# Kernel tuning notes

Measured on AMD Instinct MI355X. Metric: run time of the kernel, lower is better.

Reference implementation:

```python
import jax, jax.numpy as jnp
import numpy as np

N = 100000   # nodes
E = 3200000  # edges (before self-loops)
F = 128      # input feature dim
H = 2        # heads
C = 16       # hidden per head
G = 64       # graphs in batch
NEG_SLOPE = 0.2


def _gat_layer(x, src, dst, eattr, W, a_src, a_dst, W_e, a_e, bias):
    # x: [N, Fin]; W: [Fin, H*C]; eattr: [Et, 1]; W_e: [1, H*C]; a_*: [H, C]
    n = x.shape[0]
    h = (x @ W).reshape(n, H, C)                      # [N,H,C]
    asrc = jnp.sum(h * a_src, axis=-1)                # [N,H]
    adst = jnp.sum(h * a_dst, axis=-1)                # [N,H]
    he = (eattr @ W_e).reshape(-1, H, C)              # [Et,H,C]
    aedge = jnp.sum(he * a_e, axis=-1)                # [Et,H]
    alpha = jax.nn.leaky_relu(asrc[src] + adst[dst] + aedge, NEG_SLOPE)
    # segment softmax over incoming edges of each destination node
    m = jax.ops.segment_max(alpha, dst, num_segments=n)
    ex = jnp.exp(alpha - m[dst])
    s = jax.ops.segment_sum(ex, dst, num_segments=n)
    att = ex / (s[dst] + 1e-16)                        # [Et,H]
    msg = h[src] * att[:, :, None]                     # [Et,H,C]
    out = jax.ops.segment_sum(msg, dst, num_segments=n)  # [N,H,C]
    return out.reshape(n, H * C) + bias


def setup_inputs() -> dict:
    key = jax.random.key(0)
    ks = jax.random.split(key, 24)
    d = {
        'x': jax.random.normal(ks[0], (N, F), dtype=jnp.float32),
        'edge_index': jax.random.randint(ks[1], (2, E), 0, N, dtype=jnp.int64),
        'edge_attr': jax.random.normal(ks[2], (E, 1), dtype=jnp.float32),
        'batch': jnp.sort(jax.random.randint(ks[3], (N,), 0, G, dtype=jnp.int64)),
        # conv1: F -> H*C
        'W1': jax.random.normal(ks[4], (F, H * C), dtype=jnp.float32) * 0.1,
        'att_src1': jax.random.normal(ks[5], (H, C), dtype=jnp.float32) * 0.1,
        'att_dst1': jax.random.normal(ks[6], (H, C), dtype=jnp.float32) * 0.1,
        'We1': jax.random.normal(ks[7], (1, H * C), dtype=jnp.float32) * 0.1,
        'att_edge1': jax.random.normal(ks[8], (H, C), dtype=jnp.float32) * 0.1,
        'b1': jnp.zeros((H * C,), dtype=jnp.float32),
        # conv2: H*C -> H*C
        'W2': jax.random.normal(ks[9], (H * C, H * C), dtype=jnp.float32) * 0.1,
        'att_src2': jax.random.normal(ks[10], (H, C), dtype=jnp.float32) * 0.1,
        'att_dst2': jax.random.normal(ks[11], (H, C), dtype=jnp.float32) * 0.1,
        'We2': jax.random.normal(ks[12], (1, H * C), dtype=jnp.float32) * 0.1,
        'att_edge2': jax.random.normal(ks[13], (H, C), dtype=jnp.float32) * 0.1,
        'b2': jnp.zeros((H * C,), dtype=jnp.float32),
        # predictor MLP: 32 -> 32 -> 2
        'Wf1': jax.random.normal(ks[14], (H * C, 32), dtype=jnp.float32) * 0.1,
        'bf1': jnp.zeros((32,), dtype=jnp.float32),
        'Wf2': jax.random.normal(ks[15], (32, 2), dtype=jnp.float32) * 0.1,
        'bf2': jnp.zeros((2,), dtype=jnp.float32),
    }
    return d


def reference(x, edge_index, edge_attr, batch,
              W1, att_src1, att_dst1, We1, att_edge1, b1,
              W2, att_src2, att_dst2, We2, att_edge2, b2,
              Wf1, bf1, Wf2, bf2):
    n = x.shape[0]
    # PyG GATConv default: add self-loops with edge_attr fill_value='mean'
    loops = jnp.arange(n, dtype=edge_index.dtype)
    src = jnp.concatenate([edge_index[0], loops])
    dst = jnp.concatenate([edge_index[1], loops])
    ea = jnp.concatenate([edge_attr,
                          jnp.broadcast_to(edge_attr.mean(axis=0, keepdims=True), (n, 1))])
    h = _gat_layer(x, src, dst, ea, W1, att_src1, att_dst1, We1, att_edge1, b1)
    h = jax.nn.relu(h)  # dropout is identity in eval mode
    h = _gat_layer(h, src, dst, ea, W2, att_src2, att_dst2, We2, att_edge2, b2)
    # global mean pool over graphs
    sums = jax.ops.segment_sum(h, batch, num_segments=G)          # [G, H*C]
    cnt = jax.ops.segment_sum(jnp.ones((n,), h.dtype), batch, num_segments=G)
    emb = sums / jnp.maximum(cnt, 1.0)[:, None]
    # predictor MLP
    return jax.nn.relu(emb @ Wf1 + bf1) @ Wf2 + bf2               # [G, 2]
```

## Files before the change

kernel.cpp:

```cpp
#include <hip/hip_runtime.h>
#include <hip/hip_fp16.h>

#define N_NODES 100000
#define N_EDGES 3200000
#define F_IN    128
#define HC      32
#define CH      16
#define NGRAPH  64
#define NEG     0.2f

#define BSH   8
#define BNODE (1 << BSH)
#define NB2   ((N_NODES + BNODE - 1) >> BSH)
#define CAP   9216
#define EPB   4096
#define BTHR  1024
#define GPAD  16
#define CHK   4096
#define NPB   512
#define GSPAN 16

__device__ __forceinline__ float lrelu(float x) { return x > 0.f ? x : NEG * x; }

__device__ __forceinline__ int wscan(int v) {
#pragma unroll
    for (int off = 1; off < 64; off <<= 1) {
        int u = __shfl_up(v, off, 64);
        if ((int)(threadIdx.x & 63) >= off) v += u;
    }
    return v;
}


__global__ void k_init(int* __restrict__ gcur, float* __restrict__ params,
                       float* __restrict__ gsums) {
    int t = threadIdx.x;
    if (t < NB2) gcur[t * GPAD] = t * CAP;
    if (t < 16) params[t] = 0.f;
    gsums[t] = 0.f;
    gsums[t + 1024] = 0.f;
}


__global__ __launch_bounds__(1024)
void k_bucket(const int* __restrict__ src, const int* __restrict__ dst,
              const float* __restrict__ ea, int* __restrict__ gcur,
              int2* __restrict__ staged, float* __restrict__ params) {
    __shared__ int lcur[NB2];
    __shared__ int lscan[512];
    __shared__ int gbase[NB2];
    __shared__ int wsum[8];
    __shared__ short rbkt[EPB];
    __shared__ int2 recs[EPB];
    int t = threadIdx.x;
    int base = blockIdx.x * EPB;
    float acc = 0.f;
    for (int i = t; i < NB2; i += BTHR) lcur[i] = 0;
    __syncthreads();
    int  myb[EPB / BTHR];
    int  myrank[EPB / BTHR];
    int2 myrec[EPB / BTHR];
#pragma unroll
    for (int i = 0; i < EPB / BTHR; ++i) {
        int e = base + i * BTHR + t;
        myb[i] = -1;
        if (e < N_EDGES) {
            int dv = dst[e];
            float eav = ea[e];
            acc += eav;
            myb[i] = dv >> BSH;
            myrank[i] = atomicAdd(&lcur[myb[i]], 1);
            myrec[i] = make_int2((src[e] << BSH) | (dv & (BNODE - 1)),
                                 __float_as_int(eav));
        }
    }
    __syncthreads();
    int v = 0;
    if (t < 512) v = (t < NB2) ? lcur[t] : 0;
    int sv = wscan(v);
    if (t < 512 && (t & 63) == 63) wsum[t >> 6] = sv;
    if (t < NB2 && lcur[t] > 0) gbase[t] = atomicAdd(&gcur[t * GPAD], lcur[t]);
    __syncthreads();
    if (t < 512) {
        int bb = 0;
        for (int i = 0; i < (t >> 6); ++i) bb += wsum[i];
        lscan[t] = sv + bb;
    }
    __syncthreads();
#pragma unroll
    for (int i = 0; i < EPB / BTHR; ++i) {
        if (myb[i] >= 0) {
            int p = lscan[myb[i]] - lcur[myb[i]] + myrank[i];
            recs[p] = myrec[i];
            rbkt[p] = (short)myb[i];
        }
    }
    __syncthreads();
    int tot = lscan[511];
    for (int p = t; p < tot; p += BTHR) {
        int b = rbkt[p];
        int ex = lscan[b] - lcur[b];
        staged[gbase[b] + (p - ex)] = recs[p];
    }
    for (int m = 32; m >= 1; m >>= 1) acc += __shfl_xor(acc, m, 64);
    __shared__ float sh[BTHR / 64];
    int lane = t & 63, wid = t >> 6;
    if (lane == 0) sh[wid] = acc;
    __syncthreads();
    if (t == 0) {
        float s = 0.f;
        for (int i = 0; i < BTHR / 64; ++i) s += sh[i];
        unsafeAtomicAdd(&params[0], s);
    }
}


__global__ void k_setup(const float* __restrict__ We1, const float* __restrict__ ae1,
                        const float* __restrict__ We2, const float* __restrict__ ae2,
                        float* __restrict__ params, const int* __restrict__ gcur,
                        int* __restrict__ gstart, int* __restrict__ rowptr) {
    int t = threadIdx.x;
    if (t < 2) {
        float c1 = 0.f, c2 = 0.f;
        for (int c = 0; c < CH; ++c) {
            c1 += We1[t * CH + c] * ae1[t * CH + c];
            c2 += We2[t * CH + c] * ae2[t * CH + c];
        }
        params[2 + t] = c1;
        params[4 + t] = c2;
        if (t == 0) params[1] = params[0] / (float)N_EDGES;
    }
    __shared__ int sh[256];
    int v[2];
    int s = 0;
    for (int j = 0; j < 2; ++j) {
        int i = t * 2 + j;
        v[j] = (i < NB2) ? (gcur[i * GPAD] - i * CAP) : 0;
        s += v[j];
    }
    sh[t] = s;
    __syncthreads();
    for (int off = 1; off < 256; off <<= 1) {
        int u = (t >= off) ? sh[t - off] : 0;
        __syncthreads();
        sh[t] += u;
        __syncthreads();
    }
    int ex = sh[t] - s;
    for (int j = 0; j < 2; ++j) {
        int i = t * 2 + j;
        if (i < NB2) { gstart[i] = ex; ex += v[j]; }
    }
    if (t == 255) {
        gstart[NB2] = N_EDGES;
        rowptr[N_NODES] = N_EDGES;
    }
}


__global__ __launch_bounds__(1024)
void k_scatter(const int2* __restrict__ staged, const int* __restrict__ gcur,
               const int* __restrict__ gstart,
               int* __restrict__ rowptr, int* __restrict__ eidx,
               __half* __restrict__ eea) {
    __shared__ int cntl[BNODE];
    __shared__ int cur[BNODE];
    __shared__ int cchist[BNODE];
    __shared__ int cexcl[BNODE];
    __shared__ int ws4[4];
    __shared__ short rbkt[CHK];
    __shared__ int2 recs[CHK];
    int b = blockIdx.x, t = threadIdx.x;
    int nbase = b << BSH;
    int bcount = N_NODES - nbase;
    if (bcount > BNODE) bcount = BNODE;
    int sbase = b * CAP;
    int en = gcur[b * GPAD];
    int st_true = gstart[b];
    if (t < BNODE) cntl[t] = 0;
    __syncthreads();
    for (int e = sbase + t; e < en; e += 1024)
        atomicAdd(&cntl[staged[e].x & (BNODE - 1)], 1);
    __syncthreads();
    {
        int v = (t < BNODE) ? cntl[t] : 0;
        int sv = wscan(v);
        if (t < BNODE && (t & 63) == 63) ws4[t >> 6] = sv;
        __syncthreads();
        if (t < BNODE) {
            int bb = 0;
            for (int i = 0; i < (t >> 6); ++i) bb += ws4[i];
            int ex = st_true + sv + bb - v;
            cur[t] = ex;
            if (t < bcount) rowptr[nbase + t] = ex;
        }
        __syncthreads();
    }
    int count = en - sbase;
    for (int cb = 0; cb < count; cb += CHK) {
        int clen = count - cb;
        if (clen > CHK) clen = CHK;
        if (t < BNODE) cchist[t] = 0;
        __syncthreads();
        int  mylo[CHK / 1024];
        int  myrank[CHK / 1024];
        int2 myrec[CHK / 1024];
#pragma unroll
        for (int i = 0; i < CHK / 1024; ++i) {
            int p = i * 1024 + t;
            mylo[i] = -1;
            if (p < clen) {
                int2 r = staged[sbase + cb + p];
                mylo[i] = r.x & (BNODE - 1);
                myrank[i] = atomicAdd(&cchist[mylo[i]], 1);
                myrec[i] = r;
            }
        }
        __syncthreads();
        {
            int v = (t < BNODE) ? cchist[t] : 0;
            int sv = wscan(v);
            if (t < BNODE && (t & 63) == 63) ws4[t >> 6] = sv;
            __syncthreads();
            if (t < BNODE) {
                int bb = 0;
                for (int i = 0; i < (t >> 6); ++i) bb += ws4[i];
                cexcl[t] = sv + bb - v;
            }
            __syncthreads();
        }
#pragma unroll
        for (int i = 0; i < CHK / 1024; ++i) {
            if (mylo[i] >= 0) {
                int p = cexcl[mylo[i]] + myrank[i];
                recs[p] = myrec[i];
                rbkt[p] = (short)mylo[i];
            }
        }
        __syncthreads();
        for (int p = t; p < clen; p += 1024) {
            int lo = rbkt[p];
            int pos = cur[lo] + (p - cexcl[lo]);
            int2 r = recs[p];
            eidx[pos] = r.x;
            eea[pos] = __float2half(__int_as_float(r.y));
        }
        __syncthreads();
        if (t < BNODE) cur[t] += cchist[t];
        __syncthreads();
    }
}


#define COLS(ac, xv)                                                     \
    ac[0] = fmaf(xv.x, w0.x, ac[0]); ac[1] = fmaf(xv.x, w0.y, ac[1]);    \
    ac[2] = fmaf(xv.x, w0.z, ac[2]); ac[3] = fmaf(xv.x, w0.w, ac[3]);    \
    ac[0] = fmaf(xv.y, w1.x, ac[0]); ac[1] = fmaf(xv.y, w1.y, ac[1]);    \
    ac[2] = fmaf(xv.y, w1.z, ac[2]); ac[3] = fmaf(xv.y, w1.w, ac[3]);    \
    ac[0] = fmaf(xv.z, w2.x, ac[0]); ac[1] = fmaf(xv.z, w2.y, ac[1]);    \
    ac[2] = fmaf(xv.z, w2.z, ac[2]); ac[3] = fmaf(xv.z, w2.w, ac[3]);    \
    ac[0] = fmaf(xv.w, w3.x, ac[0]); ac[1] = fmaf(xv.w, w3.y, ac[1]);    \
    ac[2] = fmaf(xv.w, w3.z, ac[2]); ac[3] = fmaf(xv.w, w3.w, ac[3]);

template <int FIN>
__global__ __launch_bounds__(256)
void k_linear(const float* __restrict__ x, const float* __restrict__ W,
              const float* __restrict__ a_src, const float* __restrict__ a_dst,
              __half* __restrict__ h16, float* __restrict__ asrc,
              float* __restrict__ adst) {
    constexpr int PAD = FIN + 4;
    __shared__ float ws[FIN * HC];
    __shared__ float xs[64 * PAD];
    int t = threadIdx.x;
    int nbase = blockIdx.x * 64;
    int bcount = N_NODES - nbase;
    if (bcount > 64) bcount = 64;

    for (int i = t; i < FIN * HC / 4; i += 256)
        ((float4*)ws)[i] = ((const float4*)W)[i];
    const float4* xg = (const float4*)(x + (size_t)nbase * FIN);
    int nf4 = bcount * FIN / 4;
    for (int i = t; i < 64 * FIN / 4; i += 256) {
        if (i < nf4) {
            float4 v = xg[i];
            int flat = i * 4;
            int row = flat / FIN, col = flat % FIN;
            *(float4*)&xs[row * PAD + col] = v;
        }
    }
    __syncthreads();

    int cg = t & 7, np = t >> 3;
    int n0 = np * 2, n1 = n0 + 1;
    float acc0[4] = {0.f, 0.f, 0.f, 0.f};
    float acc1[4] = {0.f, 0.f, 0.f, 0.f};
#pragma unroll
    for (int k = 0; k < FIN; k += 4) {
        float4 xa = *(const float4*)&xs[n0 * PAD + k];
        float4 xb = *(const float4*)&xs[n1 * PAD + k];
        const float4* wp = (const float4*)&ws[k * HC] + cg;
        float4 w0 = wp[0], w1 = wp[8], w2 = wp[16], w3 = wp[24];
        COLS(acc0, xa)
        COLS(acc1, xb)
    }

    int hh = cg >> 2;
    float s0 = 0.f, d0 = 0.f, s1 = 0.f, d1 = 0.f;
#pragma unroll
    for (int j = 0; j < 4; ++j) {
        float av = a_src[hh * CH + (cg & 3) * 4 + j];
        float dv = a_dst[hh * CH + (cg & 3) * 4 + j];
        s0 = fmaf(acc0[j], av, s0); d0 = fmaf(acc0[j], dv, d0);
        s1 = fmaf(acc1[j], av, s1); d1 = fmaf(acc1[j], dv, d1);
    }
    s0 += __shfl_xor(s0, 1, 64); s0 += __shfl_xor(s0, 2, 64);
    d0 += __shfl_xor(d0, 1, 64); d0 += __shfl_xor(d0, 2, 64);
    s1 += __shfl_xor(s1, 1, 64); s1 += __shfl_xor(s1, 2, 64);
    d1 += __shfl_xor(d1, 1, 64); d1 += __shfl_xor(d1, 2, 64);

    if (n0 < bcount) {
        __half2 pa = __floats2half2_rn(acc0[0], acc0[1]);
        __half2 pb = __floats2half2_rn(acc0[2], acc0[3]);
        *(uint2*)&h16[(size_t)(nbase + n0) * HC + cg * 4] =
            make_uint2(*(unsigned*)&pa, *(unsigned*)&pb);
        if ((cg & 3) == 0) {
            asrc[(nbase + n0) * 2 + hh] = s0;
            adst[(nbase + n0) * 2 + hh] = d0;
        }
    }
    if (n1 < bcount) {
        __half2 pa = __floats2half2_rn(acc1[0], acc1[1]);
        __half2 pb = __floats2half2_rn(acc1[2], acc1[3]);
        *(uint2*)&h16[(size_t)(nbase + n1) * HC + cg * 4] =
            make_uint2(*(unsigned*)&pa, *(unsigned*)&pb);
        if ((cg & 3) == 0) {
            asrc[(nbase + n1) * 2 + hh] = s1;
            adst[(nbase + n1) * 2 + hh] = d1;
        }
    }
}


#define FMA4(ACC, WGT, VEC)                                                      \
    ACC.x = fmaf(WGT, VEC.x, ACC.x); ACC.y = fmaf(WGT, VEC.y, ACC.y);            \
    ACC.z = fmaf(WGT, VEC.z, ACC.z); ACC.w = fmaf(WGT, VEC.w, ACC.w);

__device__ __forceinline__ void unpack8(uint4 hv, float4& p, float4& u) {
    float2 f0 = __half22float2(*(__half2*)&hv.x);
    float2 f1 = __half22float2(*(__half2*)&hv.y);
    float2 f2 = __half22float2(*(__half2*)&hv.z);
    float2 f3 = __half22float2(*(__half2*)&hv.w);
    p = make_float4(f0.x, f0.y, f1.x, f1.y);
    u = make_float4(f2.x, f2.y, f3.x, f3.y);
}

template <int FUSE>
__global__ __launch_bounds__(256)
void k_gat(const int* __restrict__ rowptr, const int* __restrict__ eidx,
           const __half* __restrict__ eea, const __half* __restrict__ h16,
           const float* __restrict__ asrc, const float* __restrict__ adst,
           const float* __restrict__ params, int ceoff,
           const float* __restrict__ bias, int do_relu,
           float* __restrict__ outf, __half* __restrict__ outh,
           const float* __restrict__ W2,
           const float* __restrict__ as2, const float* __restrict__ ad2,
           float* __restrict__ asrc2, float* __restrict__ adst2) {
    __shared__ float w2s[FUSE ? HC * HC : 4];
    int t = threadIdx.x;
    if (FUSE) {
        for (int i = t; i < HC * HC / 4; i += 256)
            ((float4*)w2s)[i] = ((const float4*)W2)[i];
        __syncthreads();
    }
    int tid = blockIdx.x * blockDim.x + t;
    int n = tid >> 4;
    if (n >= N_NODES) return;
    int q = tid & 15;
    int chan = q & 3, quarter = q >> 2, hh = chan >> 1;
    int st = rowptr[n], en = rowptr[n + 1];
    int len = en - st;
    int q0 = st + ((len * quarter) >> 2);
    int q1 = st + ((len * (quarter + 1)) >> 2);
    float ce = params[ceoff + hh];
    float adn = adst[n * 2 + hh];
    const uint4* h4v = (const uint4*)h16;
    float4 A0 = make_float4(0.f, 0.f, 0.f, 0.f);
    float4 A1 = make_float4(0.f, 0.f, 0.f, 0.f);
    float ssum = 0.f;
    for (int e = q0; e < q1; e += 4) {
        int e1 = e + 1, e2 = e + 2, e3 = e + 3;
        int i1 = e1 < q1 ? e1 : q1 - 1;
        int i2 = e2 < q1 ? e2 : q1 - 1;
        int i3 = e3 < q1 ? e3 : q1 - 1;
        int r0 = eidx[e], r1 = eidx[i1], r2 = eidx[i2], r3 = eidx[i3];
        float ea0 = __half2float(eea[e]),  ea1 = __half2float(eea[i1]);
        float ea2 = __half2float(eea[i2]), ea3 = __half2float(eea[i3]);
        int s0 = r0 >> BSH, s1 = r1 >> BSH, s2 = r2 >> BSH, s3 = r3 >> BSH;
        float a0 = asrc[s0 * 2 + hh], a1 = asrc[s1 * 2 + hh];
        float a2 = asrc[s2 * 2 + hh], a3 = asrc[s3 * 2 + hh];
        uint4 hv0 = h4v[s0 * 4 + chan];
        uint4 hv1 = h4v[s1 * 4 + chan];
        uint4 hv2 = h4v[s2 * 4 + chan];
        uint4 hv3 = h4v[s3 * 4 + chan];
        float g0 = __expf(lrelu(a0 + adn + ce * ea0));
        float g1 = __expf(lrelu(a1 + adn + ce * ea1));
        float g2 = __expf(lrelu(a2 + adn + ce * ea2));
        float g3 = __expf(lrelu(a3 + adn + ce * ea3));
        g1 = (e1 < q1) ? g1 : 0.f;
        g2 = (e2 < q1) ? g2 : 0.f;
        g3 = (e3 < q1) ? g3 : 0.f;
        float4 p0, u0, p1, u1, p2, u2, p3, u3;
        unpack8(hv0, p0, u0); unpack8(hv1, p1, u1);
        unpack8(hv2, p2, u2); unpack8(hv3, p3, u3);
        FMA4(A0, g0, p0) FMA4(A1, g0, u0) ssum += g0;
        FMA4(A0, g1, p1) FMA4(A1, g1, u1) ssum += g1;
        FMA4(A0, g2, p2) FMA4(A1, g2, u2) ssum += g2;
        FMA4(A0, g3, p3) FMA4(A1, g3, u3) ssum += g3;
    }
    if (quarter == 0) {
        float gself = __expf(lrelu(asrc[n * 2 + hh] + adn + ce * params[1]));
        float4 psf, usf;
        unpack8(h4v[n * 4 + chan], psf, usf);
        FMA4(A0, gself, psf) FMA4(A1, gself, usf)
        ssum += gself;
    }
    A0.x += __shfl_xor(A0.x, 4, 64); A0.y += __shfl_xor(A0.y, 4, 64);
    A0.z += __shfl_xor(A0.z, 4, 64); A0.w += __shfl_xor(A0.w, 4, 64);
    A1.x += __shfl_xor(A1.x, 4, 64); A1.y += __shfl_xor(A1.y, 4, 64);
    A1.z += __shfl_xor(A1.z, 4, 64); A1.w += __shfl_xor(A1.w, 4, 64);
    ssum += __shfl_xor(ssum, 4, 64);
    A0.x += __shfl_xor(A0.x, 8, 64); A0.y += __shfl_xor(A0.y, 8, 64);
    A0.z += __shfl_xor(A0.z, 8, 64); A0.w += __shfl_xor(A0.w, 8, 64);
    A1.x += __shfl_xor(A1.x, 8, 64); A1.y += __shfl_xor(A1.y, 8, 64);
    A1.z += __shfl_xor(A1.z, 8, 64); A1.w += __shfl_xor(A1.w, 8, 64);
    ssum += __shfl_xor(ssum, 8, 64);
    if (quarter != 0) return;
    float inv = 1.f / (ssum + 1e-16f);
    int b4 = chan * 2;
    float4 bv0 = ((const float4*)bias)[b4], bv1 = ((const float4*)bias)[b4 + 1];
    float4 v0 = make_float4(A0.x * inv + bv0.x, A0.y * inv + bv0.y,
                            A0.z * inv + bv0.z, A0.w * inv + bv0.w);
    float4 v1 = make_float4(A1.x * inv + bv1.x, A1.y * inv + bv1.y,
                            A1.z * inv + bv1.z, A1.w * inv + bv1.w);
    if (do_relu) {
        v0.x = fmaxf(v0.x, 0.f); v0.y = fmaxf(v0.y, 0.f);
        v0.z = fmaxf(v0.z, 0.f); v0.w = fmaxf(v0.w, 0.f);
        v1.x = fmaxf(v1.x, 0.f); v1.y = fmaxf(v1.y, 0.f);
        v1.z = fmaxf(v1.z, 0.f); v1.w = fmaxf(v1.w, 0.f);
    }
    if (!FUSE) {
        ((float4*)outf)[n * 8 + b4] = v0;
        ((float4*)outf)[n * 8 + b4 + 1] = v1;
        return;
    }
    int lane = t & 63;
    int bse = lane & 48;
    float h2[8] = {0.f, 0.f, 0.f, 0.f, 0.f, 0.f, 0.f, 0.f};
#pragma unroll
    for (int cc = 0; cc < 4; ++cc) {
        int sl = bse | cc;
        float vv[8];
        vv[0] = __shfl(v0.x, sl, 64); vv[1] = __shfl(v0.y, sl, 64);
        vv[2] = __shfl(v0.z, sl, 64); vv[3] = __shfl(v0.w, sl, 64);
        vv[4] = __shfl(v1.x, sl, 64); vv[5] = __shfl(v1.y, sl, 64);
        vv[6] = __shfl(v1.z, sl, 64); vv[7] = __shfl(v1.w, sl, 64);
#pragma unroll
        for (int m = 0; m < 8; ++m) {
            const float* wrow = &w2s[(cc * 8 + m) * HC + chan * 8];
            float4 wa = *(const float4*)&wrow[0];
            float4 wb = *(const float4*)&wrow[4];
            h2[0] = fmaf(vv[m], wa.x, h2[0]); h2[1] = fmaf(vv[m], wa.y, h2[1]);
            h2[2] = fmaf(vv[m], wa.z, h2[2]); h2[3] = fmaf(vv[m], wa.w, h2[3]);
            h2[4] = fmaf(vv[m], wb.x, h2[4]); h2[5] = fmaf(vv[m], wb.y, h2[5]);
            h2[6] = fmaf(vv[m], wb.z, h2[6]); h2[7] = fmaf(vv[m], wb.w, h2[7]);
        }
    }
    __half2 q0h = __floats2half2_rn(h2[0], h2[1]);
    __half2 q1h = __floats2half2_rn(h2[2], h2[3]);
    __half2 q2h = __floats2half2_rn(h2[4], h2[5]);
    __half2 q3h = __floats2half2_rn(h2[6], h2[7]);
    *(uint4*)&outh[(size_t)n * HC + chan * 8] =
        make_uint4(*(unsigned*)&q0h, *(unsigned*)&q1h,
                   *(unsigned*)&q2h, *(unsigned*)&q3h);
    float s2 = 0.f, d2 = 0.f;
#pragma unroll
    for (int j = 0; j < 8; ++j) {
        s2 = fmaf(h2[j], as2[chan * 8 + j], s2);
        d2 = fmaf(h2[j], ad2[chan * 8 + j], d2);
    }
    s2 += __shfl_xor(s2, 1, 64);
    d2 += __shfl_xor(d2, 1, 64);
    if ((chan & 1) == 0) {
        asrc2[n * 2 + (chan >> 1)] = s2;
        adst2[n * 2 + (chan >> 1)] = d2;
    }
}


__global__ __launch_bounds__(1024)
void k_pool1(const float* __restrict__ feat, const int* __restrict__ batch,
             float* __restrict__ gsums) {
    __shared__ float gsum[GSPAN][32];
    int t = threadIdx.x;
    int c = t & 31, r = t >> 5;
    int base = blockIdx.x * NPB;
    if (t < GSPAN * 32) ((float*)gsum)[t] = 0.f;
    __syncthreads();
    int g0 = batch[base];
    float acc = 0.f;
    int gprev = -1;
    for (int i = 0; i < NPB / 32; ++i) {
        int n = base + r * (NPB / 32) + i;
        if (n >= N_NODES) break;
        int g = batch[n] - g0;
        if (g != gprev) {
            if (gprev >= 0) {
                if (gprev < GSPAN) atomicAdd(&gsum[gprev][c], acc);
                else unsafeAtomicAdd(&gsums[(g0 + gprev) * 32 + c], acc);
            }
            acc = 0.f;
            gprev = g;
        }
        acc += feat[(size_t)n * HC + c];
    }
    if (gprev >= 0) {
        if (gprev < GSPAN) atomicAdd(&gsum[gprev][c], acc);
        else unsafeAtomicAdd(&gsums[(g0 + gprev) * 32 + c], acc);
    }
    __syncthreads();
    if (t < GSPAN * 32) {
        int gi = t >> 5, cc = t & 31;
        float v = gsum[gi][cc];
        if (v != 0.f && g0 + gi < NGRAPH)
            unsafeAtomicAdd(&gsums[(g0 + gi) * 32 + cc], v);
    }
}


__global__ void k_mlp(const float* __restrict__ gsums, const int* __restrict__ batch,
                      const float* __restrict__ Wf1, const float* __restrict__ bf1,
                      const float* __restrict__ Wf2, const float* __restrict__ bf2,
                      float* __restrict__ out) {
    int g = blockIdx.x;
    __shared__ int sse[2];
    __shared__ float emb[32];
    __shared__ float hid[32];
    if (threadIdx.x < 2) {
        int target = g + (int)threadIdx.x;
        int lo = 0, hi = N_NODES;
        while (lo < hi) {
            int mid = (lo + hi) >> 1;
            if (batch[mid] < target) lo = mid + 1; else hi = mid;
        }
        sse[threadIdx.x] = lo;
    }
    __syncthreads();
    int cnt = sse[1] - sse[0];
    if (threadIdx.x < 32)
        emb[threadIdx.x] = gsums[g * 32 + threadIdx.x] / (float)(cnt > 0 ? cnt : 1);
    __syncthreads();
    if (threadIdx.x < 32) {
        int j = threadIdx.x;
        float a = bf1[j];
        for (int k = 0; k < 32; ++k) a = fmaf(emb[k], Wf1[k * 32 + j], a);
        hid[j] = fmaxf(a, 0.f);
    }
    __syncthreads();
    if (threadIdx.x < 2) {
        int j = threadIdx.x;
        float o = bf2[j];
        for (int k = 0; k < 32; ++k) o = fmaf(hid[k], Wf2[k * 2 + j], o);
        out[g * 2 + j] = o;
    }
}

extern "C" void kernel_launch(void* const* d_in, const int* in_sizes, int n_in,
                              void* d_out, int out_size, void* d_ws, size_t ws_size,
                              hipStream_t stream) {
    const float* x   = (const float*)d_in[0];
    const int*   ei  = (const int*)d_in[1];
    const float* ea  = (const float*)d_in[2];
    const int* batch = (const int*)d_in[3];
    const float* W1  = (const float*)d_in[4];
    const float* as1 = (const float*)d_in[5];
    const float* ad1 = (const float*)d_in[6];
    const float* We1 = (const float*)d_in[7];
    const float* ae1 = (const float*)d_in[8];
    const float* b1  = (const float*)d_in[9];
    const float* W2  = (const float*)d_in[10];
    const float* as2 = (const float*)d_in[11];
    const float* ad2 = (const float*)d_in[12];
    const float* We2 = (const float*)d_in[13];
    const float* ae2 = (const float*)d_in[14];
    const float* b2  = (const float*)d_in[15];
    const float* Wf1 = (const float*)d_in[16];
    const float* bf1 = (const float*)d_in[17];
    const float* Wf2 = (const float*)d_in[18];
    const float* bf2 = (const float*)d_in[19];
    float* out = (float*)d_out;
    (void)in_sizes; (void)n_in; (void)out_size; (void)ws_size;

    const int* srcp = ei;
    const int* dstp = ei + N_EDGES;

    char* wsb = (char*)d_ws;
    size_t off = 0;
    auto alloc = [&](size_t bytes) -> char* {
        char* p = wsb + off;
        off = (off + bytes + 255) & ~(size_t)255;
        return p;
    };
    float* params = (float*)alloc(64);
    char* regA = alloc((size_t)NB2 * CAP * 8 + 4096);
    int2*  staged = (int2*)regA;
    float* feat   = (float*)regA;
    int*   eidx   = (int*)alloc((size_t)N_EDGES * 4);
    __half* eea   = (__half*)alloc((size_t)N_EDGES * 2);
    __half* h16a  = (__half*)alloc((size_t)N_NODES * HC * 2);
    __half* h16b  = (__half*)alloc((size_t)N_NODES * HC * 2);
    float* asrc   = (float*)alloc((size_t)N_NODES * 2 * 4);
    float* adst   = (float*)alloc((size_t)N_NODES * 2 * 4);
    float* asrc2  = (float*)alloc((size_t)N_NODES * 2 * 4);
    float* adst2  = (float*)alloc((size_t)N_NODES * 2 * 4);
    int*   gstart = (int*)alloc((size_t)(NB2 + 1) * 4);
    int*   gcur   = (int*)alloc((size_t)NB2 * GPAD * 4);
    int*   rowptr = (int*)alloc((size_t)(N_NODES + 1) * 4);
    float* gsums  = (float*)alloc((size_t)NGRAPH * HC * 4);

    const int nBlkB = (N_EDGES + EPB - 1) / EPB;
    const int nBlkL = (N_NODES + 63) / 64;
    const int nBlkG = (N_NODES * 16 + 255) / 256;
    const int nBlkP = (N_NODES + NPB - 1) / NPB;

    k_init<<<1, 1024, 0, stream>>>(gcur, params, gsums);
    k_bucket<<<nBlkB, BTHR, 0, stream>>>(srcp, dstp, ea, gcur, staged, params);
    k_setup<<<1, 256, 0, stream>>>(We1, ae1, We2, ae2, params, gcur, gstart, rowptr);
    k_scatter<<<NB2, 1024, 0, stream>>>(staged, gcur, gstart, rowptr, eidx, eea);

    k_linear<F_IN><<<nBlkL, 256, 0, stream>>>(x, W1, as1, ad1, h16a, asrc, adst);
    k_gat<1><<<nBlkG, 256, 0, stream>>>(rowptr, eidx, eea, h16a, asrc, adst, params, 2, b1, 1,
                                        nullptr, h16b, W2, as2, ad2, asrc2, adst2);

    k_gat<0><<<nBlkG, 256, 0, stream>>>(rowptr, eidx, eea, h16b, asrc2, adst2, params, 4, b2, 0,
                                        feat, nullptr, W2, as2, ad2, asrc2, adst2);

    k_pool1<<<nBlkP, 1024, 0, stream>>>(feat, batch, gsums);
    k_mlp<<<NGRAPH, 64, 0, stream>>>(gsums, batch, Wf1, bf1, Wf2, bf2, out);
}
```

Before: 334.0 us.

## Split staged edge records into SoA with fp16 attrs and single-pass bucket scatter

```diff
diff --git a/kernel.cpp b/kernel.cpp
--- a/kernel.cpp
+++ b/kernel.cpp
@@ -16,7 +16,6 @@
 #define EPB   4096
 #define BTHR  1024
 #define GPAD  16
-#define CHK   4096
 #define NPB   512
 #define GSPAN 16
 
@@ -45,21 +44,24 @@
 __global__ __launch_bounds__(1024)
 void k_bucket(const int* __restrict__ src, const int* __restrict__ dst,
               const float* __restrict__ ea, int* __restrict__ gcur,
-              int2* __restrict__ staged, float* __restrict__ params) {
+              int* __restrict__ sidx, __half* __restrict__ sea,
+              float* __restrict__ params) {
     __shared__ int lcur[NB2];
     __shared__ int lscan[512];
     __shared__ int gbase[NB2];
     __shared__ int wsum[8];
     __shared__ short rbkt[EPB];
-    __shared__ int2 recs[EPB];
+    __shared__ int ridx[EPB];
+    __shared__ __half rea[EPB];
     int t = threadIdx.x;
     int base = blockIdx.x * EPB;
     float acc = 0.f;
     for (int i = t; i < NB2; i += BTHR) lcur[i] = 0;
     __syncthreads();
-    int  myb[EPB / BTHR];
-    int  myrank[EPB / BTHR];
-    int2 myrec[EPB / BTHR];
+    int   myb[EPB / BTHR];
+    int   myrank[EPB / BTHR];
+    int   myidx[EPB / BTHR];
+    float myea[EPB / BTHR];
 #pragma unroll
     for (int i = 0; i < EPB / BTHR; ++i) {
         int e = base + i * BTHR + t;
@@ -70,8 +72,8 @@
             acc += eav;
             myb[i] = dv >> BSH;
             myrank[i] = atomicAdd(&lcur[myb[i]], 1);
-            myrec[i] = make_int2((src[e] << BSH) | (dv & (BNODE - 1)),
-                                 __float_as_int(eav));
+            myidx[i] = (src[e] << BSH) | (dv & (BNODE - 1));
+            myea[i] = eav;
         }
     }
     __syncthreads();
@@ -91,7 +93,8 @@
     for (int i = 0; i < EPB / BTHR; ++i) {
         if (myb[i] >= 0) {
             int p = lscan[myb[i]] - lcur[myb[i]] + myrank[i];
-            recs[p] = myrec[i];
+            ridx[p] = myidx[i];
+            rea[p] = __float2half(myea[i]);
             rbkt[p] = (short)myb[i];
         }
     }
@@ -100,7 +103,9 @@
     for (int p = t; p < tot; p += BTHR) {
         int b = rbkt[p];
         int ex = lscan[b] - lcur[b];
-        staged[gbase[b] + (p - ex)] = recs[p];
+        int gpos = gbase[b] + (p - ex);
+        sidx[gpos] = ridx[p];
+        sea[gpos] = rea[p];
     }
     for (int m = 32; m >= 1; m >>= 1) acc += __shfl_xor(acc, m, 64);
     __shared__ float sh[BTHR / 64];
@@ -159,28 +164,38 @@
 
 
 __global__ __launch_bounds__(1024)
-void k_scatter(const int2* __restrict__ staged, const int* __restrict__ gcur,
-               const int* __restrict__ gstart,
+void k_scatter(const int* __restrict__ sidx, const __half* __restrict__ sea,
+               const int* __restrict__ gcur, const int* __restrict__ gstart,
                int* __restrict__ rowptr, int* __restrict__ eidx,
                __half* __restrict__ eea) {
     __shared__ int cntl[BNODE];
-    __shared__ int cur[BNODE];
-    __shared__ int cchist[BNODE];
-    __shared__ int cexcl[BNODE];
+    __shared__ int excl[BNODE];
     __shared__ int ws4[4];
-    __shared__ short rbkt[CHK];
-    __shared__ int2 recs[CHK];
+    __shared__ int lidx[CAP];
+    __shared__ __half lea[CAP];
     int b = blockIdx.x, t = threadIdx.x;
     int nbase = b << BSH;
     int bcount = N_NODES - nbase;
     if (bcount > BNODE) bcount = BNODE;
     int sbase = b * CAP;
     int en = gcur[b * GPAD];
+    int count = en - sbase;
     int st_true = gstart[b];
     if (t < BNODE) cntl[t] = 0;
     __syncthreads();
-    for (int e = sbase + t; e < en; e += 1024)
-        atomicAdd(&cntl[staged[e].x & (BNODE - 1)], 1);
+    int    myidx[CAP / BTHR];
+    __half myea[CAP / BTHR];
+    int    myrank[CAP / BTHR];
+#pragma unroll
+    for (int i = 0; i < CAP / BTHR; ++i) {
+        int p = i * BTHR + t;
+        myrank[i] = -1;
+        if (p < count) {
+            myidx[i] = sidx[sbase + p];
+            myea[i] = sea[sbase + p];
+            myrank[i] = atomicAdd(&cntl[myidx[i] & (BNODE - 1)], 1);
+        }
+    }
     __syncthreads();
     {
         int v = (t < BNODE) ? cntl[t] : 0;
@@ -190,64 +205,25 @@
         if (t < BNODE) {
             int bb = 0;
             for (int i = 0; i < (t >> 6); ++i) bb += ws4[i];
-            int ex = st_true + sv + bb - v;
-            cur[t] = ex;
-            if (t < bcount) rowptr[nbase + t] = ex;
+            int ex = sv + bb - v;
+            excl[t] = ex;
+            if (t < bcount) rowptr[nbase + t] = st_true + ex;
         }
         __syncthreads();
     }
-    int count = en - sbase;
-    for (int cb = 0; cb < count; cb += CHK) {
-        int clen = count - cb;
-        if (clen > CHK) clen = CHK;
-        if (t < BNODE) cchist[t] = 0;
-        __syncthreads();
-        int  mylo[CHK / 1024];
-        int  myrank[CHK / 1024];
-        int2 myrec[CHK / 1024];
-#pragma unroll
-        for (int i = 0; i < CHK / 1024; ++i) {
-            int p = i * 1024 + t;
-            mylo[i] = -1;
-            if (p < clen) {
-                int2 r = staged[sbase + cb + p];
-                mylo[i] = r.x & (BNODE - 1);
-                myrank[i] = atomicAdd(&cchist[mylo[i]], 1);
-                myrec[i] = r;
-            }
-        }
-        __syncthreads();
-        {
-            int v = (t < BNODE) ? cchist[t] : 0;
-            int sv = wscan(v);
-            if (t < BNODE && (t & 63) == 63) ws4[t >> 6] = sv;
-            __syncthreads();
-            if (t < BNODE) {
-                int bb = 0;
-                for (int i = 0; i < (t >> 6); ++i) bb += ws4[i];
-                cexcl[t] = sv + bb - v;
-            }
-            __syncthreads();
-        }
-#pragma unroll
-        for (int i = 0; i < CHK / 1024; ++i) {
-            if (mylo[i] >= 0) {
-                int p = cexcl[mylo[i]] + myrank[i];
-                recs[p] = myrec[i];
-                rbkt[p] = (short)mylo[i];
-            }
-        }
-        __syncthreads();
-        for (int p = t; p < clen; p += 1024) {
-            int lo = rbkt[p];
-            int pos = cur[lo] + (p - cexcl[lo]);
-            int2 r = recs[p];
-            eidx[pos] = r.x;
-            eea[pos] = __float2half(__int_as_float(r.y));
-        }
-        __syncthreads();
-        if (t < BNODE) cur[t] += cchist[t];
-        __syncthreads();
+#pragma unroll
+    for (int i = 0; i < CAP / BTHR; ++i) {
+        if (myrank[i] >= 0) {
+            int lo = myidx[i] & (BNODE - 1);
+            int p = excl[lo] + myrank[i];
+            lidx[p] = myidx[i];
+            lea[p] = myea[i];
+        }
+    }
+    __syncthreads();
+    for (int p = t; p < count; p += BTHR) {
+        eidx[st_true + p] = lidx[p];
+        eea[st_true + p] = lea[p];
     }
 }
 
@@ -611,9 +587,10 @@
         return p;
     };
     float* params = (float*)alloc(64);
-    char* regA = alloc((size_t)NB2 * CAP * 8 + 4096);
-    int2*  staged = (int2*)regA;
+    char* regA = alloc((size_t)NB2 * CAP * 4 + 4096);
+    int*   sidx   = (int*)regA;
     float* feat   = (float*)regA;
+    __half* sea   = (__half*)alloc((size_t)NB2 * CAP * 2);
     int*   eidx   = (int*)alloc((size_t)N_EDGES * 4);
     __half* eea   = (__half*)alloc((size_t)N_EDGES * 2);
     __half* h16a  = (__half*)alloc((size_t)N_NODES * HC * 2);
@@ -633,9 +610,9 @@
     const int nBlkP = (N_NODES + NPB - 1) / NPB;
 
     k_init<<<1, 1024, 0, stream>>>(gcur, params, gsums);
-    k_bucket<<<nBlkB, BTHR, 0, stream>>>(srcp, dstp, ea, gcur, staged, params);
+    k_bucket<<<nBlkB, BTHR, 0, stream>>>(srcp, dstp, ea, gcur, sidx, sea, params);
     k_setup<<<1, 256, 0, stream>>>(We1, ae1, We2, ae2, params, gcur, gstart, rowptr);
-    k_scatter<<<NB2, 1024, 0, stream>>>(staged, gcur, gstart, rowptr, eidx, eea);
+    k_scatter<<<NB2, 1024, 0, stream>>>(sidx, sea, gcur, gstart, rowptr, eidx, eea);
 
     k_linear<F_IN><<<nBlkL, 256, 0, stream>>>(x, W1, as1, ad1, h16a, asrc, adst);
     k_gat<1><<<nBlkG, 256, 0, stream>>>(rowptr, eidx, eea, h16a, asrc, adst, params, 2, b1, 1,
```

Result: faster. 325.9 us (median of 2 runs) (-2.4%).
